# Kernel optimization log

Measured on AMD Instinct MI355X. Metric: run time of the kernel, lower is better.

## Reference

```python
import jax, jax.numpy as jnp
import numpy as np

VOCAB = 100000
D = 128
BATCH = 16384


def setup_inputs() -> dict:
    key = jax.random.key(0)
    k_idx, k_emb, k_T, k_tv, k_w, k_b = jax.random.split(key, 6)
    bound = float(np.sqrt(3.0 / D))  # matches sqrt(3/embed_size) init scale
    indices = jax.random.randint(k_idx, (BATCH,), 0, VOCAB, dtype=jnp.int64)
    w_embed = jax.random.normal(k_emb, (VOCAB, D), dtype=jnp.float32)
    T = jax.random.uniform(k_T, (D, D, D), dtype=jnp.float32, minval=-bound, maxval=bound)
    B = jnp.zeros((D, D), dtype=jnp.float32)
    time_vec = jax.random.uniform(k_tv, (D,), dtype=jnp.float32, minval=-bound, maxval=bound)
    lin_bound = 1.0 / float(np.sqrt(D))  # nn.Linear default init range
    op_w = jax.random.uniform(k_w, (D, D), dtype=jnp.float32, minval=-lin_bound, maxval=lin_bound)
    op_b = jax.random.uniform(k_b, (D,), dtype=jnp.float32, minval=-lin_bound, maxval=lin_bound)
    return {"indices": indices, "w_embed": w_embed, "T": T, "B": B,
            "time_vec": time_vec, "op_w": op_w, "op_b": op_b}


def reference(indices, w_embed, T, B, time_vec, op_w, op_b):
    # embedding lookup: [b, d]
    we = w_embed[indices]
    # trilinear contraction: [b, d] x [d, d, d] -> [b, d, d], plus bias B
    TransW = jnp.einsum('bx,xyz->byz', we, T) + B[None, :, :]
    # reduce last axis with time_vec: [b, d]
    h3 = jnp.einsum('byz,z->by', TransW, time_vec)
    # op_layer (nn.Linear): x @ W^T + b
    return h3 @ op_w.T + op_b
```

## Files before the change

### kernel.cpp

```cpp
#include <hip/hip_runtime.h>

#define D 128
#define MTILE 64
#define WPITCH 68

__global__ __launch_bounds__(128) void prep_kernel(
    const float* __restrict__ T, const float* __restrict__ Bm,
    const float* __restrict__ tv, const float* __restrict__ op_w,
    const float* __restrict__ op_b, float* __restrict__ W2,
    float* __restrict__ bias2)
{
    __shared__ float m_s[D];
    const int x = blockIdx.x;
    const int t = threadIdx.x;
    const float* src = (x < D) ? (T + (size_t)x * D * D) : Bm;
    const float4* row = (const float4*)(src + t * D);
    const float4* tv4 = (const float4*)tv;
    float acc = 0.f;
#pragma unroll 8
    for (int k = 0; k < D / 4; ++k) {
        float4 a = row[k];
        float4 b = tv4[k];
        acc += a.x * b.x + a.y * b.y + a.z * b.z + a.w * b.w;
    }
    m_s[t] = acc;
    __syncthreads();
    const float4* wrow = (const float4*)(op_w + t * D);
    const float4* m4 = (const float4*)m_s;
    float acc2 = 0.f;
#pragma unroll 8
    for (int k = 0; k < D / 4; ++k) {
        float4 a = wrow[k];
        float4 b = m4[k];
        acc2 += a.x * b.x + a.y * b.y + a.z * b.z + a.w * b.w;
    }
    if (x < D) W2[x * D + t] = acc2;
    else       bias2[t] = acc2 + op_b[t];
}

__global__ __launch_bounds__(256) void main_gemm(
    const int* __restrict__ idx, const float* __restrict__ w_embed,
    const float* __restrict__ W2, const float* __restrict__ bias2,
    float* __restrict__ out)
{
    __shared__ float weT[D][WPITCH];
    __shared__ float W2s[D * D];
    __shared__ float bias_s[D];

    const int t = threadIdx.x;
    const int b0 = blockIdx.x * MTILE;

    {
        const int r = t & 63;
        const int q = t >> 6;
        const int g = idx[b0 + r];
        const float4* src = (const float4*)(w_embed + (size_t)g * D + q * 32);
#pragma unroll
        for (int k = 0; k < 8; ++k) {
            float4 v = src[k];
            const int x = q * 32 + k * 4;
            weT[x + 0][r] = v.x;
            weT[x + 1][r] = v.y;
            weT[x + 2][r] = v.z;
            weT[x + 3][r] = v.w;
        }
    }
    {
        const float4* s = (const float4*)W2;
        float4* dst = (float4*)W2s;
#pragma unroll
        for (int i = 0; i < (D * D / 4) / 256; ++i)
            dst[t + i * 256] = s[t + i * 256];
    }
    if (t < D / 4) ((float4*)bias_s)[t] = ((const float4*)bias2)[t];
    __syncthreads();

    const int tx = t & 15;
    const int ty = t >> 4;
    const int c0 = tx * 8;
    const int r0 = ty * 4;

    float acc[4][8];
#pragma unroll
    for (int i = 0; i < 4; ++i)
#pragma unroll
        for (int j = 0; j < 8; ++j) acc[i][j] = 0.f;

#pragma unroll 4
    for (int x = 0; x < D; ++x) {
        float4 a  = *(const float4*)&weT[x][r0];
        float4 bA = *(const float4*)&W2s[x * D + c0];
        float4 bB = *(const float4*)&W2s[x * D + c0 + 4];
        const float av[4] = {a.x, a.y, a.z, a.w};
        const float bv[8] = {bA.x, bA.y, bA.z, bA.w, bB.x, bB.y, bB.z, bB.w};
#pragma unroll
        for (int i = 0; i < 4; ++i)
#pragma unroll
            for (int j = 0; j < 8; ++j)
                acc[i][j] += av[i] * bv[j];
    }

    float4 bb0 = *(const float4*)&bias_s[c0];
    float4 bb1 = *(const float4*)&bias_s[c0 + 4];
    const float bb[8] = {bb0.x, bb0.y, bb0.z, bb0.w, bb1.x, bb1.y, bb1.z, bb1.w};
#pragma unroll
    for (int i = 0; i < 4; ++i) {
        float* o = out + (size_t)(b0 + r0 + i) * D + c0;
        float4 o0 = make_float4(acc[i][0] + bb[0], acc[i][1] + bb[1],
                                acc[i][2] + bb[2], acc[i][3] + bb[3]);
        float4 o1 = make_float4(acc[i][4] + bb[4], acc[i][5] + bb[5],
                                acc[i][6] + bb[6], acc[i][7] + bb[7]);
        *(float4*)o = o0;
        *(float4*)(o + 4) = o1;
    }
}

extern "C" void kernel_launch(void* const* d_in, const int* in_sizes, int n_in,
                              void* d_out, int out_size, void* d_ws, size_t ws_size,
                              hipStream_t stream) {
    const int*   idx     = (const int*)d_in[0];
    const float* w_embed = (const float*)d_in[1];
    const float* T       = (const float*)d_in[2];
    const float* Bm      = (const float*)d_in[3];
    const float* tv      = (const float*)d_in[4];
    const float* op_w    = (const float*)d_in[5];
    const float* op_b    = (const float*)d_in[6];
    float* out = (float*)d_out;

    float* W2    = (float*)d_ws;
    float* bias2 = W2 + D * D;

    prep_kernel<<<D + 1, D, 0, stream>>>(T, Bm, tv, op_w, op_b, W2, bias2);
    main_gemm<<<16384 / MTILE, 256, 0, stream>>>(idx, w_embed, W2, bias2, out);
}
```

Measured before the change: 23.89 us.

## Replace FP32 SIMT GEMM with bf16 MFMA and split precompute into two stages

The main GEMM now uses bf16 MFMA 16x16x32 instructions, reading gathered embedding rows straight from global memory and converting them to bf16 in registers, with no shared-memory staging or barriers. The folded weight matrix is stored transposed in bf16. Precomputation is split into a row-parallel contraction of T with time_vec across many blocks, followed by a small kernel that applies op_w. This trades FP32 accuracy for bf16 operands and adds an extra kernel launch.

After: 22.38 us. 6.3% less time.

```diff
diff --git a/kernel.cpp b/kernel.cpp
--- a/kernel.cpp
+++ b/kernel.cpp
@@ -1,117 +1,105 @@
 #include <hip/hip_runtime.h>
 
 #define D 128
-#define MTILE 64
-#define WPITCH 68
+#define BATCH 16384
 
-__global__ __launch_bounds__(128) void prep_kernel(
+typedef float f32x4 __attribute__((ext_vector_type(4)));
+typedef short bh8 __attribute__((ext_vector_type(8)));
+
+__device__ __forceinline__ unsigned short f2bf(float f) {
+    unsigned u = __float_as_uint(f);
+    u += 0x7FFFu + ((u >> 16) & 1u);
+    return (unsigned short)(u >> 16);
+}
+
+__global__ __launch_bounds__(256) void stage1(
     const float* __restrict__ T, const float* __restrict__ Bm,
-    const float* __restrict__ tv, const float* __restrict__ op_w,
-    const float* __restrict__ op_b, float* __restrict__ W2,
+    const float* __restrict__ tv, float* __restrict__ m)
+{
+    const int t = threadIdx.x;
+    const int lr = t >> 5;
+    const int c4 = t & 31;
+    const int R = blockIdx.x * 8 + lr;
+    const float* src = (R < BATCH) ? (T + (size_t)R * D)
+                                   : (Bm + (size_t)(R - BATCH) * D);
+    f32x4 v = *(const f32x4*)(src + c4 * 4);
+    f32x4 w = *(const f32x4*)(tv + c4 * 4);
+    float p = v[0]*w[0] + v[1]*w[1] + v[2]*w[2] + v[3]*w[3];
+#pragma unroll
+    for (int s = 16; s >= 1; s >>= 1) p += __shfl_xor(p, s, 32);
+    if (c4 == 0) m[R] = p;
+}
+
+__global__ __launch_bounds__(128) void stage2(
+    const float* __restrict__ m, const float* __restrict__ op_w,
+    const float* __restrict__ op_b, unsigned short* __restrict__ W2T,
     float* __restrict__ bias2)
 {
-    __shared__ float m_s[D];
-    const int x = blockIdx.x;
-    const int t = threadIdx.x;
-    const float* src = (x < D) ? (T + (size_t)x * D * D) : Bm;
-    const float4* row = (const float4*)(src + t * D);
-    const float4* tv4 = (const float4*)tv;
+    __shared__ float wj[D];
+    __shared__ float red[D];
+    const int j = blockIdx.x;
+    const int x = threadIdx.x;
+    if (x < D / 4) ((f32x4*)wj)[x] = ((const f32x4*)(op_w + (size_t)j * D))[x];
+    __syncthreads();
+    const float* mr = m + (size_t)x * D;
     float acc = 0.f;
-#pragma unroll 8
+#pragma unroll
     for (int k = 0; k < D / 4; ++k) {
-        float4 a = row[k];
-        float4 b = tv4[k];
-        acc += a.x * b.x + a.y * b.y + a.z * b.z + a.w * b.w;
+        f32x4 a = ((const f32x4*)mr)[k];
+        f32x4 b = ((const f32x4*)wj)[k];
+        acc += a[0]*b[0] + a[1]*b[1] + a[2]*b[2] + a[3]*b[3];
     }
-    m_s[t] = acc;
+    W2T[(size_t)j * D + x] = f2bf(acc);
+    red[x] = m[(size_t)BATCH * 1 * 0 + 16384 + x] * wj[x];
     __syncthreads();
-    const float4* wrow = (const float4*)(op_w + t * D);
-    const float4* m4 = (const float4*)m_s;
-    float acc2 = 0.f;
-#pragma unroll 8
-    for (int k = 0; k < D / 4; ++k) {
-        float4 a = wrow[k];
-        float4 b = m4[k];
-        acc2 += a.x * b.x + a.y * b.y + a.z * b.z + a.w * b.w;
+    if (x == 0) {
+        float s = 0.f;
+        for (int y = 0; y < D; ++y) s += red[y];
+        bias2[j] = s + op_b[j];
     }
-    if (x < D) W2[x * D + t] = acc2;
-    else       bias2[t] = acc2 + op_b[t];
 }
 
-__global__ __launch_bounds__(256) void main_gemm(
-    const int* __restrict__ idx, const float* __restrict__ w_embed,
-    const float* __restrict__ W2, const float* __restrict__ bias2,
+__global__ __launch_bounds__(256) void main_mfma(
+    const int* __restrict__ idx, const float* __restrict__ we,
+    const unsigned short* __restrict__ W2T, const float* __restrict__ bias2,
     float* __restrict__ out)
 {
-    __shared__ float weT[D][WPITCH];
-    __shared__ float W2s[D * D];
-    __shared__ float bias_s[D];
+    const int t = threadIdx.x;
+    const int wv = t >> 6;
+    const int l = t & 63;
+    const int l15 = l & 15, lg = l >> 4;
+    const int b0 = (blockIdx.x * 4 + wv) * 16;
 
-    const int t = threadIdx.x;
-    const int b0 = blockIdx.x * MTILE;
+    const int g = idx[b0 + l15];
+    const float* arow = we + (size_t)g * D;
 
-    {
-        const int r = t & 63;
-        const int q = t >> 6;
-        const int g = idx[b0 + r];
-        const float4* src = (const float4*)(w_embed + (size_t)g * D + q * 32);
+    f32x4 acc[8];
 #pragma unroll
-        for (int k = 0; k < 8; ++k) {
-            float4 v = src[k];
-            const int x = q * 32 + k * 4;
-            weT[x + 0][r] = v.x;
-            weT[x + 1][r] = v.y;
-            weT[x + 2][r] = v.z;
-            weT[x + 3][r] = v.w;
+    for (int c = 0; c < 8; ++c) acc[c] = (f32x4){0.f, 0.f, 0.f, 0.f};
+
+#pragma unroll
+    for (int s = 0; s < 4; ++s) {
+        f32x4 a0 = *(const f32x4*)(arow + s * 32 + lg * 8);
+        f32x4 a1 = *(const f32x4*)(arow + s * 32 + lg * 8 + 4);
+        bh8 af;
+        af[0] = (short)f2bf(a0[0]); af[1] = (short)f2bf(a0[1]);
+        af[2] = (short)f2bf(a0[2]); af[3] = (short)f2bf(a0[3]);
+        af[4] = (short)f2bf(a1[0]); af[5] = (short)f2bf(a1[1]);
+        af[6] = (short)f2bf(a1[2]); af[7] = (short)f2bf(a1[3]);
+#pragma unroll
+        for (int c = 0; c < 8; ++c) {
+            bh8 bf = *(const bh8*)(W2T + (size_t)(c * 16 + l15) * D + s * 32 + lg * 8);
+            acc[c] = __builtin_amdgcn_mfma_f32_16x16x32_bf16(af, bf, acc[c], 0, 0, 0);
         }
     }
-    {
-        const float4* s = (const float4*)W2;
-        float4* dst = (float4*)W2s;
+
 #pragma unroll
-        for (int i = 0; i < (D * D / 4) / 256; ++i)
-            dst[t + i * 256] = s[t + i * 256];
-    }
-    if (t < D / 4) ((float4*)bias_s)[t] = ((const float4*)bias2)[t];
-    __syncthreads();
-
-    const int tx = t & 15;
-    const int ty = t >> 4;
-    const int c0 = tx * 8;
-    const int r0 = ty * 4;
-
-    float acc[4][8];
+    for (int c = 0; c < 8; ++c) {
+        float bv = bias2[c * 16 + l15];
 #pragma unroll
-    for (int i = 0; i < 4; ++i)
-#pragma unroll
-        for (int j = 0; j < 8; ++j) acc[i][j] = 0.f;
-
-#pragma unroll 4
-    for (int x = 0; x < D; ++x) {
-        float4 a  = *(const float4*)&weT[x][r0];
-        float4 bA = *(const float4*)&W2s[x * D + c0];
-        float4 bB = *(const float4*)&W2s[x * D + c0 + 4];
-        const float av[4] = {a.x, a.y, a.z, a.w};
-        const float bv[8] = {bA.x, bA.y, bA.z, bA.w, bB.x, bB.y, bB.z, bB.w};
-#pragma unroll
-        for (int i = 0; i < 4; ++i)
-#pragma unroll
-            for (int j = 0; j < 8; ++j)
-                acc[i][j] += av[i] * bv[j];
-    }
-
-    float4 bb0 = *(const float4*)&bias_s[c0];
-    float4 bb1 = *(const float4*)&bias_s[c0 + 4];
-    const float bb[8] = {bb0.x, bb0.y, bb0.z, bb0.w, bb1.x, bb1.y, bb1.z, bb1.w};
-#pragma unroll
-    for (int i = 0; i < 4; ++i) {
-        float* o = out + (size_t)(b0 + r0 + i) * D + c0;
-        float4 o0 = make_float4(acc[i][0] + bb[0], acc[i][1] + bb[1],
-                                acc[i][2] + bb[2], acc[i][3] + bb[3]);
-        float4 o1 = make_float4(acc[i][4] + bb[4], acc[i][5] + bb[5],
-                                acc[i][6] + bb[6], acc[i][7] + bb[7]);
-        *(float4*)o = o0;
-        *(float4*)(o + 4) = o1;
+        for (int r = 0; r < 4; ++r) {
+            out[(size_t)(b0 + lg * 4 + r) * D + c * 16 + l15] = acc[c][r] + bv;
+        }
     }
 }
 
@@ -127,9 +115,11 @@
     const float* op_b    = (const float*)d_in[6];
     float* out = (float*)d_out;
 
-    float* W2    = (float*)d_ws;
-    float* bias2 = W2 + D * D;
+    float* m = (float*)d_ws;
+    unsigned short* W2T = (unsigned short*)((char*)d_ws + 66048);
+    float* bias2 = (float*)((char*)d_ws + 66048 + 32768);
 
-    prep_kernel<<<D + 1, D, 0, stream>>>(T, Bm, tv, op_w, op_b, W2, bias2);
-    main_gemm<<<16384 / MTILE, 256, 0, stream>>>(idx, w_embed, W2, bias2, out);
+    stage1<<<(BATCH + D + 7) / 8, 256, 0, stream>>>(T, Bm, tv, m);
+    stage2<<<D, D, 0, stream>>>(m, op_w, op_b, W2T, bias2);
+    main_mfma<<<BATCH / 64, 256, 0, stream>>>(idx, w_embed, W2T, bias2, out);
 }
```
